# Performance work log

Hardware: AMD Instinct MI355X
Metric: run time of the kernel (lower is better)

Reference implementation:

```python
import jax, jax.numpy as jnp
import numpy as np
from jax import lax

T = 256          # sentence length
WD, TD = 300, 100  # word/tag embedding dims
H = WD + TD      # LSTM hidden (=input) size, per module __init__
VOCAB, NTAGS = 50000, 50
MLP_H = 400


def setup_inputs() -> dict:
    key = jax.random.key(0)
    ks = jax.random.split(key, 20)
    s = 0.05  # small init scale for numerical stability
    return {
        "words": jax.random.randint(ks[0], (T,), 0, VOCAB),
        "tags": jax.random.randint(ks[1], (T,), 0, NTAGS),
        "word_emb": jax.random.normal(ks[2], (VOCAB, WD), jnp.float32),
        "tag_emb": jax.random.normal(ks[3], (NTAGS, TD), jnp.float32),
        "Wih0": jax.random.normal(ks[4], (2, 4 * H, H), jnp.float32) * s,
        "Whh0": jax.random.normal(ks[5], (2, 4 * H, H), jnp.float32) * s,
        "bih0": jax.random.normal(ks[6], (2, 4 * H), jnp.float32) * s,
        "bhh0": jax.random.normal(ks[7], (2, 4 * H), jnp.float32) * s,
        "Wih1": jax.random.normal(ks[8], (2, 4 * H, 2 * H), jnp.float32) * s,
        "Whh1": jax.random.normal(ks[9], (2, 4 * H, H), jnp.float32) * s,
        "bih1": jax.random.normal(ks[10], (2, 4 * H), jnp.float32) * s,
        "bhh1": jax.random.normal(ks[11], (2, 4 * H), jnp.float32) * s,
        "W1": jax.random.normal(ks[12], (MLP_H, 4 * H), jnp.float32) * s,
        "b1": jax.random.normal(ks[13], (MLP_H,), jnp.float32) * s,
        "W2": jax.random.normal(ks[14], (1, MLP_H), jnp.float32) * s,
        "b2": jax.random.normal(ks[15], (1,), jnp.float32) * s,
        "h0": jax.random.normal(ks[16], (2, 2, H), jnp.float32),  # [layer, dir, H]
        "c0": jax.random.normal(ks[17], (2, 2, H), jnp.float32),
    }


def _lstm_dir(xs, Wih, Whh, bih, bhh, h0, c0, reverse):
    # xs: [T, D]; torch LSTM gate order i, f, g, o
    def step(carry, xt):
        h, c = carry
        g = xt @ Wih.T + bih + h @ Whh.T + bhh  # [4H]
        i, f, gg, o = jnp.split(g, 4)
        c = jax.nn.sigmoid(f) * c + jax.nn.sigmoid(i) * jnp.tanh(gg)
        h = jax.nn.sigmoid(o) * jnp.tanh(c)
        return (h, c), h
    _, hs = lax.scan(step, (h0, c0), xs, reverse=reverse)
    return hs  # [T, H]


def _forward(words, tags, word_emb, tag_emb, Wih0, Whh0, bih0, bhh0,
             Wih1, Whh1, bih1, bhh1, W1, b1, W2, b2, h0, c0):
    x = jnp.concatenate([word_emb[words], tag_emb[tags]], axis=1)  # [T, H]
    # layer 0, both directions
    hf0 = _lstm_dir(x, Wih0[0], Whh0[0], bih0[0], bhh0[0], h0[0, 0], c0[0, 0], False)
    hb0 = _lstm_dir(x, Wih0[1], Whh0[1], bih0[1], bhh0[1], h0[0, 1], c0[0, 1], True)
    x1 = jnp.concatenate([hf0, hb0], axis=1)  # [T, 2H]
    # layer 1
    hf1 = _lstm_dir(x1, Wih1[0], Whh1[0], bih1[0], bhh1[0], h0[1, 0], c0[1, 0], False)
    hb1 = _lstm_dir(x1, Wih1[1], Whh1[1], bih1[1], bhh1[1], h0[1, 1], c0[1, 1], True)
    hvec = jnp.concatenate([hf1, hb1], axis=1)  # [T, 2H]
    # batched pairwise MLP: score(i,j) = W2 @ tanh(W1 @ [h_i; h_j] + b1) + b2
    # Split W1 so the concat is never materialized over all T^2 pairs.
    W1a, W1b = W1[:, :2 * H], W1[:, 2 * H:]
    pi = hvec @ W1a.T  # [T, MLP_H] contribution of head word i
    pj = hvec @ W1b.T  # [T, MLP_H] contribution of dependent word j
    act = jnp.tanh(pi[:, None, :] + pj[None, :, :] + b1)  # [T, T, MLP_H]
    scores = act @ W2[0] + b2[0]  # [T, T]
    # diagonal stays 0 (permutations exclude i == j; scoreTensor was zeroed)
    return scores * (1.0 - jnp.eye(T, dtype=scores.dtype))


def reference(words, tags, word_emb, tag_emb, Wih0, Whh0, bih0, bhh0,
              Wih1, Whh1, bih1, bhh1, W1, b1, W2, b2, h0, c0):
    return _forward(words, tags, word_emb, tag_emb, Wih0, Whh0, bih0, bhh0,
                    Wih1, Whh1, bih1, bhh1, W1, b1, W2, b2, h0, c0)
```

## Files before the change

kernel.cpp:

```cpp
#include <hip/hip_runtime.h>
#include <hip/hip_bf16.h>

#define T 256
#define H 400
#define G4 1600
#define WD 300
#define TD 100
#define MLP_H 400
#define NBLK 25
#define HB 16
#define GR 64
#define WSTR 202
#define NPAIR 200

typedef _Float16 f16;
typedef _Float16 half2t __attribute__((ext_vector_type(2)));
typedef unsigned long long u64;
typedef unsigned int u32;

__device__ __forceinline__ float fexp(float x) {
    return __builtin_amdgcn_exp2f(x * 1.4426950408889634f);
}
__device__ __forceinline__ float sigf(float x) {
    return __builtin_amdgcn_rcpf(1.0f + fexp(-x));
}
__device__ __forceinline__ float tanhf_fast(float x) {
    return 1.0f - 2.0f * __builtin_amdgcn_rcpf(1.0f + fexp(2.0f * x));
}
__device__ __forceinline__ unsigned short f16bits(f16 x) {
    union { f16 h; unsigned short u; } v; v.h = x; return v.u;
}
__device__ __forceinline__ u32 packh2(float a, float b) {
    half2t hv; hv.x = (_Float16)a; hv.y = (_Float16)b;
    return __builtin_bit_cast(u32, hv);
}

#if __has_builtin(__builtin_amdgcn_fdot2)
__device__ __forceinline__ float dot2u(u32 a, u32 b, float c) {
    return __builtin_amdgcn_fdot2(__builtin_bit_cast(half2t, a),
                                  __builtin_bit_cast(half2t, b), c, false);
}
#else
__device__ __forceinline__ float dot2u(u32 a, u32 b, float c) {
    half2t x = __builtin_bit_cast(half2t, a), y = __builtin_bit_cast(half2t, b);
    return fmaf((float)x.y, (float)y.y, fmaf((float)x.x, (float)y.x, c));
}
#endif

__device__ __forceinline__ u64 sysload(const u64* p) {
    return __hip_atomic_load(p, __ATOMIC_RELAXED, __HIP_MEMORY_SCOPE_SYSTEM);
}
__device__ __forceinline__ void sysstore(u64* p, u64 v) {
    __hip_atomic_store(p, v, __ATOMIC_RELAXED, __HIP_MEMORY_SCOPE_SYSTEM);
}

__global__ void gather_k(const int* __restrict__ words, const int* __restrict__ tags,
                         const float* __restrict__ wemb, const float* __restrict__ temb,
                         float* __restrict__ x0) {
    int t = blockIdx.x;
    int w = words[t], g = tags[t];
    for (int c = threadIdx.x; c < H; c += 128) {
        float v = (c < WD) ? wemb[w * WD + c] : temb[g * TD + (c - WD)];
        x0[t * H + c] = v;
    }
}

__global__ __launch_bounds__(256) void gemm_tn(
    const float* __restrict__ X, int ldx,
    const float* __restrict__ Wt, int ldw, int wofs,
    const float* __restrict__ bias1, const float* __restrict__ bias2,
    float* __restrict__ out, int ldo, int Rt, int K) {
    __shared__ float Xs[64][17];
    __shared__ float Ws[64][17];
    const int tid = threadIdx.x;
    const int t0 = blockIdx.x * 64, r0 = blockIdx.y * 64;
    const int lr = tid >> 2, kq = (tid & 3) * 4;
    const int ti = tid >> 4, rj = tid & 15;
    float acc[4][4] = {};
    for (int k0 = 0; k0 < K; k0 += 16) {
        float4 xv = *(const float4*)(X + (size_t)(t0 + lr) * ldx + k0 + kq);
        Xs[lr][kq + 0] = xv.x; Xs[lr][kq + 1] = xv.y;
        Xs[lr][kq + 2] = xv.z; Xs[lr][kq + 3] = xv.w;
        int r = r0 + lr;
        float4 wv = make_float4(0.f, 0.f, 0.f, 0.f);
        if (r < Rt) wv = *(const float4*)(Wt + (size_t)r * ldw + wofs + k0 + kq);
        Ws[lr][kq + 0] = wv.x; Ws[lr][kq + 1] = wv.y;
        Ws[lr][kq + 2] = wv.z; Ws[lr][kq + 3] = wv.w;
        __syncthreads();
#pragma unroll
        for (int k = 0; k < 16; k++) {
            float xr[4], wr[4];
#pragma unroll
            for (int m = 0; m < 4; m++) xr[m] = Xs[ti * 4 + m][k];
#pragma unroll
            for (int n = 0; n < 4; n++) wr[n] = Ws[rj * 4 + n][k];
#pragma unroll
            for (int m = 0; m < 4; m++)
#pragma unroll
                for (int n = 0; n < 4; n++)
                    acc[m][n] = fmaf(xr[m], wr[n], acc[m][n]);
        }
        __syncthreads();
    }
    int rq = r0 + rj * 4;
    if (rq < Rt) {
        float b[4];
#pragma unroll
        for (int n = 0; n < 4; n++) {
            int r = rq + n;
            b[n] = (bias1 ? bias1[r] : 0.f) + (bias2 ? bias2[r] : 0.f);
        }
#pragma unroll
        for (int m = 0; m < 4; m++) {
            int t = t0 + ti * 4 + m;
            float4 o;
            o.x = acc[m][0] + b[0]; o.y = acc[m][1] + b[1];
            o.z = acc[m][2] + b[2]; o.w = acc[m][3] + b[3];
            *(float4*)(out + (size_t)t * ldo + rq) = o;
        }
    }
}

__global__ void lstm_init5(const float* __restrict__ h0, u64* sA, u64* sB) {
    int tid = threadIdx.x;
    const int TOT = 2 * 2 * NPAIR;
    for (int i = tid; i < TOT; i += 256) { sA[i] = 0xFFFFULL; sB[i] = 0xFFFFULL; }
    __syncthreads();
    for (int p = tid; p < 2 * NPAIR; p += 256) {
        int d = p / NPAIR, pr = p - d * NPAIR;
        size_t off = (size_t)(d * 2 + 0) * NPAIR + pr;
        f16 a0 = (f16)h0[d * H + 2 * pr], b0 = (f16)h0[d * H + 2 * pr + 1];
        sA[off] = 0ULL | ((u64)f16bits(a0) << 16) | ((u64)f16bits(b0) << 32);
        f16 a1 = (f16)h0[2 * H + d * H + 2 * pr], b1 = (f16)h0[2 * H + d * H + 2 * pr + 1];
        sB[off] = 0ULL | ((u64)f16bits(a1) << 16) | ((u64)f16bits(b1) << 32);
    }
}

__global__ __launch_bounds__(512, 1) void lstm_layer_dual(
    const float* __restrict__ G,
    const float* __restrict__ Whh,
    const float* __restrict__ c0l,
    float* __restrict__ xout,
    u64* __restrict__ slots) {
    const int blk = blockIdx.x;
    const int tid = threadIdx.x;
    u64* sdF = slots;
    u64* sdB = slots + 2 * NPAIR;

    __shared__ u32 wlds[2][GR * WSTR];
    __shared__ __align__(16) u32 hshF[NPAIR];
    __shared__ __align__(16) u32 hshB[NPAIR];
    __shared__ float gsum[GR];
    __shared__ float gshF[2][GR];
    __shared__ float gshB[2][GR];

    for (int idx = tid; idx < 2 * GR * 100; idx += 512) {
        int d = idx / (GR * 100), rem = idx - d * (GR * 100);
        int row = rem / 100, c4 = rem - row * 100;
        int g = row >> 4, r = row & 15;
        const float4* src = (const float4*)(
            Whh + (size_t)d * G4 * H + (size_t)(g * H + blk * HB + r) * H);
        float4 f = src[c4];
        *(uint2*)&wlds[d][row * WSTR + c4 * 2] =
            make_uint2(packh2(f.x, f.y), packh2(f.z, f.w));
    }
    if (tid >= 448) {
        int i = tid - 448, gg = i >> 4, rr = i & 15;
        gshF[0][i] = G[(size_t)0 * G4 + gg * H + blk * HB + rr];
        gshB[0][i] = G[((size_t)T + (T - 1)) * G4 + gg * H + blk * HB + rr];
    } else if (tid < 8) {
        u64 v = sysload(sdF + blk * 8 + tid);
        hshF[blk * 8 + tid] = (u32)(v >> 16);
    } else if (tid < 16) {
        u64 v = sysload(sdB + blk * 8 + (tid - 8));
        hshB[blk * 8 + (tid - 8)] = (u32)(v >> 16);
    } else if (tid >= 256 && tid < 448) {
        int f = tid - 256;
        int widx = f + (f >= blk * 8 ? 8 : 0);
        u64* src = sdF + widx;
        u64 v = sysload(src);
        int spins = 0;
        while ((unsigned)(v & 0xFFFFULL) != 0u) {
            if (++spins > 16384) {
                v = __hip_atomic_fetch_add(src, 0ULL, __ATOMIC_RELAXED,
                                           __HIP_MEMORY_SCOPE_AGENT);
            } else {
                v = sysload(src);
            }
        }
        hshF[widx] = (u32)(v >> 16);
    }
    float cf = (tid < 64) ? c0l[blk * HB + (tid & 15)] : 0.f;
    float cb = (tid < 64) ? c0l[H + blk * HB + (tid & 15)] : 0.f;
    __syncthreads();

#pragma clang loop unroll(disable)
    for (int s = 0; s < T; ++s) {
#pragma clang loop unroll(disable)
        for (int d = 0; d < 2; ++d) {
            if (tid >= 256 && tid < 448) {
                int f = tid - 256;
                int widx = f + (f >= blk * 8 ? 8 : 0);
                int tg = (d == 0) ? s : (s + 1);
                if (tg < T) {
                    u64* src = (d == 0 ? sdB : sdF) + (size_t)(tg & 1) * NPAIR + widx;
                    u64 v = sysload(src);
                    int spins = 0;
                    while ((unsigned)(v & 0xFFFFULL) != (unsigned)tg) {
                        if (++spins > 16384) {
                            v = __hip_atomic_fetch_add(src, 0ULL, __ATOMIC_RELAXED,
                                                       __HIP_MEMORY_SCOPE_AGENT);
                        } else {
                            v = sysload(src);
                        }
                    }
                    (d == 0 ? hshB : hshF)[widx] = (u32)(v >> 16);
                }
            } else if (tid >= 448) {
                int sn = (s + 1 < T) ? (s + 1) : s;
                int tt = d ? (T - 1 - sn) : sn;
                int i = tid - 448, gg = i >> 4, rr = i & 15;
                (d ? gshB : gshF)[(s + 1) & 1][i] =
                    G[((size_t)d * T + tt) * G4 + gg * H + blk * HB + rr];
            } else {
                const int row = tid >> 2, sl = tid & 3;
                const u32* wp = &wlds[d][row * WSTR + sl * 50];
                const u32* hp = &(d ? hshB : hshF)[sl * 50];
                float a0 = 0.f, a1 = 0.f, a2 = 0.f, a3 = 0.f;
#pragma unroll
                for (int i = 0; i < 12; ++i) {
                    uint2 wv0 = *(const uint2*)&wp[4 * i];
                    uint2 hv0 = *(const uint2*)&hp[4 * i];
                    uint2 wv1 = *(const uint2*)&wp[4 * i + 2];
                    uint2 hv1 = *(const uint2*)&hp[4 * i + 2];
                    a0 = dot2u(wv0.x, hv0.x, a0);
                    a1 = dot2u(wv0.y, hv0.y, a1);
                    a2 = dot2u(wv1.x, hv1.x, a2);
                    a3 = dot2u(wv1.y, hv1.y, a3);
                }
                {
                    uint2 wv = *(const uint2*)&wp[48];
                    uint2 hv = *(const uint2*)&hp[48];
                    a0 = dot2u(wv.x, hv.x, a0);
                    a1 = dot2u(wv.y, hv.y, a1);
                }
                float a = (a0 + a1) + (a2 + a3);
                a += __shfl_xor(a, 1);
                a += __shfl_xor(a, 2);
                if (sl == 0) gsum[row] = a;
            }
            __syncthreads();

            if (tid < 64) {
                const int r = tid & 15;
                const float* gc = (d ? gshB : gshF)[s & 1];
                float iv = gsum[r]      + gc[r];
                float fv = gsum[16 + r] + gc[16 + r];
                float gv = gsum[32 + r] + gc[32 + r];
                float ov = gsum[48 + r] + gc[48 + r];
                float c = d ? cb : cf;
                float cn = sigf(fv) * c + sigf(iv) * tanhf_fast(gv);
                if (d) cb = cn; else cf = cn;
                float hn = sigf(ov) * tanhf_fast(cn);
                u32 hb = (u32)f16bits((f16)hn);
                u32 lo = __shfl(hb, (2 * tid) & 63);
                u32 hi = __shfl(hb, (2 * tid + 1) & 63);
                if (tid < 8) {
                    u32 pk = (lo & 0xFFFFu) | (hi << 16);
                    (d ? hshB : hshF)[blk * 8 + tid] = pk;
                    sysstore((d ? sdB : sdF) + (size_t)((s + 1) & 1) * NPAIR + blk * 8 + tid,
                             (u64)(unsigned)(s + 1) | ((u64)pk << 16));
                }
                const int tt = d ? (T - 1 - s) : s;
                if (tid < 16)
                    xout[(size_t)tt * (2 * H) + d * H + blk * HB + tid] = hn;
            }
            __syncthreads();
        }
    }
}

__global__ __launch_bounds__(256) void scores_k(
    const float* __restrict__ pi, const float* __restrict__ pj,
    const float* __restrict__ w2, const float* __restrict__ b2p,
    float* __restrict__ out) {
    __shared__ float Ps[16][401];
    __shared__ float Qs[16][401];
    __shared__ float w2s[400];
    const int tid = threadIdx.x;
    const int i0 = blockIdx.y * 16, j0 = blockIdx.x * 16;
    for (int r = 0; r < 16; r++) {
        for (int k = tid; k < MLP_H; k += 256) {
            Ps[r][k] = pi[(size_t)(i0 + r) * MLP_H + k];
            Qs[r][k] = pj[(size_t)(j0 + r) * MLP_H + k];
        }
    }
    for (int k = tid; k < MLP_H; k += 256) w2s[k] = w2[k];
    __syncthreads();
    const int ti = tid >> 4, tj = tid & 15;
    float acc = 0.f;
#pragma unroll 4
    for (int k = 0; k < MLP_H; k++) {
        float x = Ps[ti][k] + Qs[tj][k];
        acc = fmaf(w2s[k], tanhf_fast(x), acc);
    }
    const int i = i0 + ti, j = j0 + tj;
    out[(size_t)i * T + j] = (i == j) ? 0.f : (acc + b2p[0]);
}

extern "C" void kernel_launch(void* const* d_in, const int* in_sizes, int n_in,
                              void* d_out, int out_size, void* d_ws, size_t ws_size,
                              hipStream_t stream) {
    const int*   words = (const int*)d_in[0];
    const int*   tags  = (const int*)d_in[1];
    const float* wemb  = (const float*)d_in[2];
    const float* temb  = (const float*)d_in[3];
    const float* Wih0  = (const float*)d_in[4];
    const float* Whh0  = (const float*)d_in[5];
    const float* bih0  = (const float*)d_in[6];
    const float* bhh0  = (const float*)d_in[7];
    const float* Wih1  = (const float*)d_in[8];
    const float* Whh1  = (const float*)d_in[9];
    const float* bih1  = (const float*)d_in[10];
    const float* bhh1  = (const float*)d_in[11];
    const float* W1    = (const float*)d_in[12];
    const float* b1    = (const float*)d_in[13];
    const float* W2    = (const float*)d_in[14];
    const float* b2    = (const float*)d_in[15];
    const float* h0    = (const float*)d_in[16];
    const float* c0    = (const float*)d_in[17];
    float* out = (float*)d_out;

    float* W = (float*)d_ws;
    float* x0   = W;
    float* x1   = W + 102400;
    float* hvec = W + 307200;
    float* Gb   = W + 512000;
    float* pi   = W + 1331200;
    float* pj   = W + 1433600;
    u64* slotsA = (u64*)W;
    u64* slotsB = (u64*)(W + 2048);

    gather_k<<<T, 128, 0, stream>>>(words, tags, wemb, temb, x0);

    for (int d = 0; d < 2; d++) {
        gemm_tn<<<dim3(4, 25), 256, 0, stream>>>(
            x0, H, Wih0 + (size_t)d * G4 * H, H, 0,
            bih0 + d * G4, bhh0 + d * G4,
            Gb + (size_t)d * T * G4, G4, G4, H);
    }
    lstm_init5<<<1, 256, 0, stream>>>(h0, slotsA, slotsB);
    lstm_layer_dual<<<NBLK, 512, 0, stream>>>(Gb, Whh0, c0, x1, slotsA);

    for (int d = 0; d < 2; d++) {
        gemm_tn<<<dim3(4, 25), 256, 0, stream>>>(
            x1, 2 * H, Wih1 + (size_t)d * G4 * (2 * H), 2 * H, 0,
            bih1 + d * G4, bhh1 + d * G4,
            Gb + (size_t)d * T * G4, G4, G4, 2 * H);
    }
    lstm_layer_dual<<<NBLK, 512, 0, stream>>>(Gb, Whh1, c0 + 2 * H, hvec, slotsB);

    gemm_tn<<<dim3(4, 7), 256, 0, stream>>>(
        hvec, 2 * H, W1, G4, 0, b1, nullptr, pi, MLP_H, MLP_H, 2 * H);
    gemm_tn<<<dim3(4, 7), 256, 0, stream>>>(
        hvec, 2 * H, W1, G4, 2 * H, nullptr, nullptr, pj, MLP_H, MLP_H, 2 * H);

    scores_k<<<dim3(16, 16), 256, 0, stream>>>(pi, pj, W2, b2, out);
}
```

Baseline: 1.536 ms.

## Software-pipeline LSTM dual-direction steps with one barrier per phase

```diff
diff --git a/kernel.cpp b/kernel.cpp
--- a/kernel.cpp
+++ b/kernel.cpp
@@ -150,9 +150,7 @@
     __shared__ u32 wlds[2][GR * WSTR];
     __shared__ __align__(16) u32 hshF[NPAIR];
     __shared__ __align__(16) u32 hshB[NPAIR];
-    __shared__ float gsum[GR];
-    __shared__ float gshF[2][GR];
-    __shared__ float gshB[2][GR];
+    __shared__ float gsum[2][GR];
 
     for (int idx = tid; idx < 2 * GR * 100; idx += 512) {
         int d = idx / (GR * 100), rem = idx - d * (GR * 100);
@@ -164,10 +162,17 @@
         *(uint2*)&wlds[d][row * WSTR + c4 * 2] =
             make_uint2(packh2(f.x, f.y), packh2(f.z, f.w));
     }
+    float cf = 0.f, cb = 0.f;
+    float gFi = 0.f, gFf = 0.f, gFg = 0.f, gFo = 0.f;
+    float gBi = 0.f, gBf = 0.f, gBg = 0.f, gBo = 0.f;
     if (tid >= 448) {
-        int i = tid - 448, gg = i >> 4, rr = i & 15;
-        gshF[0][i] = G[(size_t)0 * G4 + gg * H + blk * HB + rr];
-        gshB[0][i] = G[((size_t)T + (T - 1)) * G4 + gg * H + blk * HB + rr];
+        int L = tid - 448, r = L & 15;
+        cf = c0l[blk * HB + r];
+        cb = c0l[H + blk * HB + r];
+        const float* gp0 = G + blk * HB + r;
+        gFi = gp0[0]; gFf = gp0[H]; gFg = gp0[2 * H]; gFo = gp0[3 * H];
+        const float* gp1 = G + ((size_t)T + (T - 1)) * G4 + blk * HB + r;
+        gBi = gp1[0]; gBf = gp1[H]; gBg = gp1[2 * H]; gBo = gp1[3 * H];
     } else if (tid < 8) {
         u64 v = sysload(sdF + blk * 8 + tid);
         hshF[blk * 8 + tid] = (u32)(v >> 16);
@@ -190,42 +195,16 @@
         }
         hshF[widx] = (u32)(v >> 16);
     }
-    float cf = (tid < 64) ? c0l[blk * HB + (tid & 15)] : 0.f;
-    float cb = (tid < 64) ? c0l[H + blk * HB + (tid & 15)] : 0.f;
     __syncthreads();
 
 #pragma clang loop unroll(disable)
-    for (int s = 0; s < T; ++s) {
-#pragma clang loop unroll(disable)
-        for (int d = 0; d < 2; ++d) {
-            if (tid >= 256 && tid < 448) {
-                int f = tid - 256;
-                int widx = f + (f >= blk * 8 ? 8 : 0);
-                int tg = (d == 0) ? s : (s + 1);
-                if (tg < T) {
-                    u64* src = (d == 0 ? sdB : sdF) + (size_t)(tg & 1) * NPAIR + widx;
-                    u64 v = sysload(src);
-                    int spins = 0;
-                    while ((unsigned)(v & 0xFFFFULL) != (unsigned)tg) {
-                        if (++spins > 16384) {
-                            v = __hip_atomic_fetch_add(src, 0ULL, __ATOMIC_RELAXED,
-                                                       __HIP_MEMORY_SCOPE_AGENT);
-                        } else {
-                            v = sysload(src);
-                        }
-                    }
-                    (d == 0 ? hshB : hshF)[widx] = (u32)(v >> 16);
-                }
-            } else if (tid >= 448) {
-                int sn = (s + 1 < T) ? (s + 1) : s;
-                int tt = d ? (T - 1 - sn) : sn;
-                int i = tid - 448, gg = i >> 4, rr = i & 15;
-                (d ? gshB : gshF)[(s + 1) & 1][i] =
-                    G[((size_t)d * T + tt) * G4 + gg * H + blk * HB + rr];
-            } else {
+    for (int p = 0; p <= 2 * T; ++p) {
+        if (tid < 256) {
+            if (p < 2 * T) {
+                const int d = p & 1;
                 const int row = tid >> 2, sl = tid & 3;
                 const u32* wp = &wlds[d][row * WSTR + sl * 50];
-                const u32* hp = &(d ? hshB : hshF)[sl * 50];
+                const u32* hp = (d ? hshB : hshF) + sl * 50;
                 float a0 = 0.f, a1 = 0.f, a2 = 0.f, a3 = 0.f;
 #pragma unroll
                 for (int i = 0; i < 12; ++i) {
@@ -247,36 +226,61 @@
                 float a = (a0 + a1) + (a2 + a3);
                 a += __shfl_xor(a, 1);
                 a += __shfl_xor(a, 2);
-                if (sl == 0) gsum[row] = a;
+                if (sl == 0) gsum[d][row] = a;
             }
-            __syncthreads();
-
-            if (tid < 64) {
-                const int r = tid & 15;
-                const float* gc = (d ? gshB : gshF)[s & 1];
-                float iv = gsum[r]      + gc[r];
-                float fv = gsum[16 + r] + gc[16 + r];
-                float gv = gsum[32 + r] + gc[32 + r];
-                float ov = gsum[48 + r] + gc[48 + r];
-                float c = d ? cb : cf;
-                float cn = sigf(fv) * c + sigf(iv) * tanhf_fast(gv);
-                if (d) cb = cn; else cf = cn;
-                float hn = sigf(ov) * tanhf_fast(cn);
-                u32 hb = (u32)f16bits((f16)hn);
-                u32 lo = __shfl(hb, (2 * tid) & 63);
-                u32 hi = __shfl(hb, (2 * tid + 1) & 63);
-                if (tid < 8) {
-                    u32 pk = (lo & 0xFFFFu) | (hi << 16);
-                    (d ? hshB : hshF)[blk * 8 + tid] = pk;
-                    sysstore((d ? sdB : sdF) + (size_t)((s + 1) & 1) * NPAIR + blk * 8 + tid,
-                             (u64)(unsigned)(s + 1) | ((u64)pk << 16));
+        } else if (tid < 448) {
+            int dd, tg;
+            if (p & 1) { dd = 0; tg = ((p - 1) >> 1) + 1; }
+            else       { dd = 1; tg = p >> 1; }
+            if (tg < T) {
+                int f = tid - 256;
+                int widx = f + (f >= blk * 8 ? 8 : 0);
+                u64* src = (dd ? sdB : sdF) + (size_t)(tg & 1) * NPAIR + widx;
+                u64 v = sysload(src);
+                int spins = 0;
+                while ((unsigned)(v & 0xFFFFULL) != (unsigned)tg) {
+                    if (++spins > 16384) {
+                        v = __hip_atomic_fetch_add(src, 0ULL, __ATOMIC_RELAXED,
+                                                   __HIP_MEMORY_SCOPE_AGENT);
+                    } else {
+                        v = sysload(src);
+                    }
                 }
-                const int tt = d ? (T - 1 - s) : s;
-                if (tid < 16)
-                    xout[(size_t)tt * (2 * H) + d * H + blk * HB + tid] = hn;
+                (dd ? hshB : hshF)[widx] = (u32)(v >> 16);
             }
-            __syncthreads();
-        }
+        } else if (p >= 1) {
+            const int L = tid - 448, r = L & 15;
+            const int d = (p & 1) ? 0 : 1;
+            const int s = (p & 1) ? ((p - 1) >> 1) : ((p - 2) >> 1);
+            float iv, fv, gv, ov, c;
+            if (d == 0) { iv = gFi; fv = gFf; gv = gFg; ov = gFo; c = cf; }
+            else        { iv = gBi; fv = gBf; gv = gBg; ov = gBo; c = cb; }
+            iv += gsum[d][r];
+            fv += gsum[d][16 + r];
+            gv += gsum[d][32 + r];
+            ov += gsum[d][48 + r];
+            float cn = sigf(fv) * c + sigf(iv) * tanhf_fast(gv);
+            if (d == 0) cf = cn; else cb = cn;
+            float hn = sigf(ov) * tanhf_fast(cn);
+            u32 hb = (u32)f16bits((f16)hn);
+            u32 lo = __shfl(hb, (2 * L) & 63);
+            u32 hi = __shfl(hb, (2 * L + 1) & 63);
+            if (L < 8) {
+                u32 pk = (lo & 0xFFFFu) | (hi << 16);
+                (d ? hshB : hshF)[blk * 8 + L] = pk;
+                sysstore((d ? sdB : sdF) + (size_t)((s + 1) & 1) * NPAIR + blk * 8 + L,
+                         (u64)(unsigned)(s + 1) | ((u64)pk << 16));
+            }
+            const int tt = d ? (T - 1 - s) : s;
+            if (L < 16)
+                xout[(size_t)tt * (2 * H) + d * H + blk * HB + L] = hn;
+            int sn = (s + 1 < T) ? (s + 1) : s;
+            int ttn = d ? (T - 1 - sn) : sn;
+            const float* gp = G + ((size_t)d * T + ttn) * G4 + blk * HB + r;
+            if (d == 0) { gFi = gp[0]; gFf = gp[H]; gFg = gp[2 * H]; gFo = gp[3 * H]; }
+            else        { gBi = gp[0]; gBf = gp[H]; gBg = gp[2 * H]; gBo = gp[3 * H]; }
+        }
+        __syncthreads();
     }
 }
 
```

New measurement: 1.894 ms. 23.3% more time.
